# Kernel tuning notes

Measured on AMD Instinct MI355X. Metric: run time of the kernel, lower is better.

## Reference

```python
import jax, jax.numpy as jnp
import numpy as np

N = 262144   # number of samples (graph edges)
D = 32       # in_features; 'delta_t' is column 0
H = D - 1    # hidden width of each bucket MLP
K = 21       # number of time buckets


def setup_inputs() -> dict:
    key = jax.random.key(0)
    ks = jax.random.split(key, 7)
    x = jax.random.uniform(ks[0], (N, D), dtype=jnp.float32)
    x = x.at[:, 0].set(x[:, 0] * 2.1)  # delta_t in (0, 2.1] -> hits all 21 buckets
    s = 1.0 / np.sqrt(H).astype(np.float32)
    a = jax.random.normal(ks[1], (H,), jnp.float32)           # FeatureTransform scale a_i
    b = jax.random.normal(ks[2], (H,), jnp.float32) * 0.1     # FeatureTransform bias b_i
    W1 = jax.random.normal(ks[3], (K, H, H), jnp.float32) * s # layer_blocks weights
    b1 = jax.random.normal(ks[4], (K, H), jnp.float32) * s
    W2 = jax.random.normal(ks[5], (K, H), jnp.float32) * s    # layer_blocks2 weights (out=1)
    b2 = jax.random.normal(ks[6], (K,), jnp.float32) * s
    return {"x": x, "a": a, "b": b, "W1": W1, "b1": b1, "W2": W2, "b2": b2}


def reference(x, a, b, W1, b1, W2, b2):
    # delta_t column is NOT feature-transformed; all other columns are.
    # Note: the torch code mutates x in place, so x_without_t sees the
    # transformed features while t is the raw delta_t.
    t = x[:, 0]                                   # [N]
    feats = x[:, 1:] * a + b                      # FeatureTransform: a_i*x_i + b_i, [N,H]
    # All 21 bucket branches: Linear -> LeakyReLU(0.1) -> Linear(H,1)
    h = jnp.einsum('nd,kde->kne', feats, W1) + b1[:, None, :]   # [K,N,H]
    h = jnp.where(h >= 0, h, 0.1 * h)                           # LeakyReLU(0.1)
    out = jnp.einsum('kne,ke->kn', h, W2) + b2[:, None]         # [K,N]
    # bucket mask: start < t <= end with edges 0.0,0.1,...,2.0,1000
    edges = jnp.concatenate([jnp.arange(K, dtype=jnp.float32) / 10.0,
                             jnp.array([1000.0], dtype=jnp.float32)])
    valid = (t[None, :] > edges[:-1, None]) & (t[None, :] <= edges[1:, None])  # [K,N]
    return (out * valid.astype(out.dtype)).sum(axis=0)[:, None]  # [N,1]
```

## Files before the change

kernel.cpp:

```cpp
#include <hip/hip_runtime.h>
#include <hip/hip_bf16.h>

#define NN 262144
#define DD 32
#define HH 31
#define KK 21
#define ROWS 128
#define FSTRIDE 18

typedef __attribute__((ext_vector_type(8))) short bf16x8;
typedef __attribute__((ext_vector_type(4))) float f32x4;
typedef __attribute__((ext_vector_type(2))) unsigned int u32x2;
typedef __attribute__((ext_vector_type(4))) unsigned int u32x4;

static __device__ __forceinline__ unsigned short f2bf(float f) {
    __hip_bfloat16 h = __float2bfloat16(f);
    return __builtin_bit_cast(unsigned short, h);
}
static __device__ __forceinline__ unsigned pack2(float lo, float hi) {
    return (unsigned)f2bf(lo) | ((unsigned)f2bf(hi) << 16);
}

__global__ __launch_bounds__(64) void prep_kernel(
    const float* __restrict__ W1, const float* __restrict__ b1,
    const float* __restrict__ W2,
    bf16x8* __restrict__ A0tab, bf16x8* __restrict__ A1tab,
    f32x4* __restrict__ cq0b, f32x4* __restrict__ cq0w,
    f32x4* __restrict__ cq1b, f32x4* __restrict__ cq1w)
{
    const int k = (int)blockIdx.x;
    const int lane = (int)threadIdx.x;
    const int lrow = lane & 15, lgrp = lane >> 4;
    const float* __restrict__ W1k = W1 + k * HH * HH;
    const int e0 = lrow, e1 = 16 + lrow;

    bf16x8 A0, A1;
    #pragma unroll
    for (int j = 0; j < 4; ++j) {
        const int d1 = 4 * lgrp + j;
        const int d2 = 16 + 4 * lgrp + j;
        A0[j]     = (short)f2bf(W1k[d1 * HH + e0]);
        A0[4 + j] = (d2 < HH) ? (short)f2bf(W1k[d2 * HH + e0]) : (short)0;
        A1[j]     = (e1 < HH) ? (short)f2bf(W1k[d1 * HH + e1]) : (short)0;
        A1[4 + j] = (e1 < HH && d2 < HH) ? (short)f2bf(W1k[d2 * HH + e1]) : (short)0;
    }
    A0tab[k * 64 + lane] = A0;
    A1tab[k * 64 + lane] = A1;

    f32x4 b0v, w0v, b1v, w1v;
    #pragma unroll
    for (int r = 0; r < 4; ++r) {
        const int e = 4 * lgrp + r, eb = 16 + e;
        b0v[r] = b1[k * HH + e];
        w0v[r] = W2[k * HH + e];
        b1v[r] = (eb < HH) ? b1[k * HH + eb] : 0.0f;
        w1v[r] = (eb < HH) ? W2[k * HH + eb] : 0.0f;
    }
    cq0b[k * 64 + lane] = b0v;
    cq0w[k * 64 + lane] = w0v;
    cq1b[k * 64 + lane] = b1v;
    cq1w[k * 64 + lane] = w1v;
}

__global__ __launch_bounds__(256, 8) void fused_kernel(
    const float* __restrict__ x,
    const float* __restrict__ a,
    const float* __restrict__ b,
    const float* __restrict__ b2,
    const bf16x8* __restrict__ A0tab, const bf16x8* __restrict__ A1tab,
    const f32x4* __restrict__ cq0b, const f32x4* __restrict__ cq0w,
    const f32x4* __restrict__ cq1b, const f32x4* __restrict__ cq1w,
    float* __restrict__ out)
{
    __shared__ unsigned fbf[ROWS * FSTRIDE];
    __shared__ int cnt[KK];
    __shared__ int rnk[KK];
    __shared__ int sbase[KK];
    __shared__ int tstart[KK + 1];
    __shared__ unsigned short sorted[ROWS];

    const int tid = (int)threadIdx.x;
    const int lane = tid & 63;
    const int rowbase = (int)blockIdx.x * ROWS;

    if (tid < KK) { cnt[tid] = 0; rnk[tid] = 0; }
    __syncthreads();

    const int r    = tid >> 1;
    const int half = tid & 1;
    const float4* __restrict__ p =
        reinterpret_cast<const float4*>(x) + (size_t)blockIdx.x * (ROWS * DD / 4) + tid * 4;
    float4 c[4];
    #pragma unroll
    for (int i = 0; i < 4; ++i) c[i] = p[i];

    const float e16 = __shfl(c[0].x, lane + 1);

    const float t = c[0].x;
    const float edges[KK + 1] = {
        0.0f, 0.1f, 0.2f, 0.3f, 0.4f, 0.5f, 0.6f, 0.7f, 0.8f, 0.9f, 1.0f,
        1.1f, 1.2f, 1.3f, 1.4f, 1.5f, 1.6f, 1.7f, 1.8f, 1.9f, 2.0f, 1000.0f
    };
    int kq = -1;
    #pragma unroll
    for (int j = 0; j < KK; ++j)
        if (t > edges[j] && t <= edges[j + 1]) kq = j;

    unsigned* __restrict__ frow = fbf + r * FSTRIDE + half * 8;
    if (half == 0) {
        float f[16];
        #pragma unroll
        for (int j = 0; j < 15; ++j) {
            const float xe = (j + 1 < 4)  ? ((j + 1 == 1) ? c[0].y : (j + 1 == 2) ? c[0].z : c[0].w)
                                          : ((const float*)c)[j + 1];
            f[j] = fmaf(xe, a[j], b[j]);
        }
        f[15] = fmaf(e16, a[15], b[15]);
        #pragma unroll
        for (int s = 0; s < 8; ++s) frow[s] = pack2(f[2 * s], f[2 * s + 1]);
    } else {
        float f[16];
        #pragma unroll
        for (int j = 0; j < 15; ++j) {
            const float xe = ((const float*)c)[j + 1];
            f[j] = fmaf(xe, a[16 + j], b[16 + j]);
        }
        f[15] = 0.0f;
        #pragma unroll
        for (int s = 0; s < 8; ++s) frow[s] = pack2(f[2 * s], f[2 * s + 1]);
    }

    if (half == 0) {
        if (kq >= 0) atomicAdd(&cnt[kq], 1);
        else out[rowbase + r] = 0.0f;
    }
    __syncthreads();

    if (tid < 64) {
        const int j = tid;
        const int c0 = (j < KK) ? cnt[j] : 0;
        const int t0 = (j < KK) ? ((c0 + 15) >> 4) : 0;
        int sc = c0, st = t0;
        #pragma unroll
        for (int off = 1; off < 32; off <<= 1) {
            const int vc = __shfl_up(sc, off);
            const int vt = __shfl_up(st, off);
            if (j >= off) { sc += vc; st += vt; }
        }
        if (j < KK) { sbase[j] = sc - c0; tstart[j] = st - t0; }
        if (j == KK) tstart[KK] = st;
    }
    __syncthreads();
    if (half == 0 && kq >= 0) {
        const int rr = atomicAdd(&rnk[kq], 1);
        sorted[sbase[kq] + rr] = (unsigned short)r;
    }
    __syncthreads();

    const int wave = tid >> 6;
    const int lrow = lane & 15;
    const int lgrp = lane >> 4;

    const int NT = tstart[KK];
    const int ts_l = tstart[(lane <= KK) ? lane : KK];

    for (int tix = wave; tix < NT; tix += 4) {
        const unsigned long long m = __ballot(ts_l <= tix);
        const int k = __builtin_amdgcn_readfirstlane(__popcll(m) - 1);

        const int sb = sbase[k];
        const int cn = cnt[k];
        const int r0 = (tix - tstart[k]) * 16;
        const int rl = r0 + lrow;

        const int R = sorted[sb + ((rl < cn) ? rl : 0)];

        const unsigned* __restrict__ fr = fbf + R * FSTRIDE;
        const u32x2 wlo = *(const u32x2*)(fr + 2 * lgrp);
        const u32x2 whi = *(const u32x2*)(fr + 8 + 2 * lgrp);
        u32x4 bw;
        bw[0] = wlo[0]; bw[1] = wlo[1]; bw[2] = whi[0]; bw[3] = whi[1];
        const bf16x8 B = __builtin_bit_cast(bf16x8, bw);

        const bf16x8 A0 = A0tab[k * 64 + lane];
        const bf16x8 A1 = A1tab[k * 64 + lane];
        const f32x4 cb0 = cq0b[k * 64 + lane];
        const f32x4 cw0 = cq0w[k * 64 + lane];
        const f32x4 cb1 = cq1b[k * 64 + lane];
        const f32x4 cw1 = cq1w[k * 64 + lane];
        const float b2k = b2[k];

        f32x4 acc0 = {0.0f, 0.0f, 0.0f, 0.0f};
        f32x4 acc1 = {0.0f, 0.0f, 0.0f, 0.0f};
        acc0 = __builtin_amdgcn_mfma_f32_16x16x32_bf16(A0, B, acc0, 0, 0, 0);
        acc1 = __builtin_amdgcn_mfma_f32_16x16x32_bf16(A1, B, acc1, 0, 0, 0);

        float S = 0.0f;
        #pragma unroll
        for (int rr = 0; rr < 4; ++rr) {
            const float h0 = acc0[rr] + cb0[rr];
            const float q0 = (h0 >= 0.0f) ? h0 : 0.1f * h0;
            S = fmaf(q0, cw0[rr], S);
            const float h1 = acc1[rr] + cb1[rr];
            const float q1 = (h1 >= 0.0f) ? h1 : 0.1f * h1;
            S = fmaf(q1, cw1[rr], S);
        }
        S += __shfl_xor(S, 16);
        S += __shfl_xor(S, 32);

        if (lgrp == 0 && rl < cn) out[rowbase + R] = S + b2k;
    }
}

extern "C" void kernel_launch(void* const* d_in, const int* in_sizes, int n_in,
                              void* d_out, int out_size, void* d_ws, size_t ws_size,
                              hipStream_t stream) {
    const float* x  = (const float*)d_in[0];
    const float* a  = (const float*)d_in[1];
    const float* b  = (const float*)d_in[2];
    const float* W1 = (const float*)d_in[3];
    const float* b1 = (const float*)d_in[4];
    const float* W2 = (const float*)d_in[5];
    const float* b2 = (const float*)d_in[6];
    float* out = (float*)d_out;

    char* ws = (char*)d_ws;
    bf16x8* A0tab = (bf16x8*)ws;
    bf16x8* A1tab = A0tab + KK * 64;
    f32x4* cq0b = (f32x4*)(A1tab + KK * 64);
    f32x4* cq0w = cq0b + KK * 64;
    f32x4* cq1b = cq0w + KK * 64;
    f32x4* cq1w = cq1b + KK * 64;

    hipLaunchKernelGGL(prep_kernel, dim3(KK), dim3(64), 0, stream,
                       W1, b1, W2, A0tab, A1tab, cq0b, cq0w, cq1b, cq1w);

    hipLaunchKernelGGL(fused_kernel, dim3(NN / ROWS), dim3(256), 0, stream,
                       x, a, b, b2, A0tab, A1tab, cq0b, cq0w, cq1b, cq1w, out);
}
```

Baseline: 22.66 us.

## Stage all bucket weights in LDS per block and double rows per block

The prep kernel now writes a padded bf16 transposed W1 table plus a bias/W2 table. Each fused block copies all 21 buckets' weights (about 48KB) into shared memory and builds its MFMA A fragments from LDS rather than from per-lane global loads. ROWS grows from 128 to 256, so each block sorts and processes twice as many rows, which spreads the weight-staging cost over more work. The catch is much larger LDS use per block (occupancy hint drops to 2), a serial weight copy at block start, and half as many blocks (1024).

```diff
diff --git a/kernel.cpp b/kernel.cpp
--- a/kernel.cpp
+++ b/kernel.cpp
@@ -5,8 +5,12 @@
 #define DD 32
 #define HH 31
 #define KK 21
-#define ROWS 128
+#define ROWS 256
 #define FSTRIDE 18
+#define WROW 36
+#define WK (32 * WROW)
+#define W1BF_B (KK * WK * 2)
+#define BW2_F (KK * 64)
 
 typedef __attribute__((ext_vector_type(8))) short bf16x8;
 typedef __attribute__((ext_vector_type(4))) float f32x4;
@@ -21,58 +25,39 @@
     return (unsigned)f2bf(lo) | ((unsigned)f2bf(hi) << 16);
 }
 
-__global__ __launch_bounds__(64) void prep_kernel(
+__global__ __launch_bounds__(256) void prep_kernel(
     const float* __restrict__ W1, const float* __restrict__ b1,
     const float* __restrict__ W2,
-    bf16x8* __restrict__ A0tab, bf16x8* __restrict__ A1tab,
-    f32x4* __restrict__ cq0b, f32x4* __restrict__ cq0w,
-    f32x4* __restrict__ cq1b, f32x4* __restrict__ cq1w)
+    unsigned short* __restrict__ gW1bf, float* __restrict__ gbw2)
 {
     const int k = (int)blockIdx.x;
-    const int lane = (int)threadIdx.x;
-    const int lrow = lane & 15, lgrp = lane >> 4;
-    const float* __restrict__ W1k = W1 + k * HH * HH;
-    const int e0 = lrow, e1 = 16 + lrow;
-
-    bf16x8 A0, A1;
-    #pragma unroll
-    for (int j = 0; j < 4; ++j) {
-        const int d1 = 4 * lgrp + j;
-        const int d2 = 16 + 4 * lgrp + j;
-        A0[j]     = (short)f2bf(W1k[d1 * HH + e0]);
-        A0[4 + j] = (d2 < HH) ? (short)f2bf(W1k[d2 * HH + e0]) : (short)0;
-        A1[j]     = (e1 < HH) ? (short)f2bf(W1k[d1 * HH + e1]) : (short)0;
-        A1[4 + j] = (e1 < HH && d2 < HH) ? (short)f2bf(W1k[d2 * HH + e1]) : (short)0;
-    }
-    A0tab[k * 64 + lane] = A0;
-    A1tab[k * 64 + lane] = A1;
-
-    f32x4 b0v, w0v, b1v, w1v;
-    #pragma unroll
-    for (int r = 0; r < 4; ++r) {
-        const int e = 4 * lgrp + r, eb = 16 + e;
-        b0v[r] = b1[k * HH + e];
-        w0v[r] = W2[k * HH + e];
-        b1v[r] = (eb < HH) ? b1[k * HH + eb] : 0.0f;
-        w1v[r] = (eb < HH) ? W2[k * HH + eb] : 0.0f;
-    }
-    cq0b[k * 64 + lane] = b0v;
-    cq0w[k * 64 + lane] = w0v;
-    cq1b[k * 64 + lane] = b1v;
-    cq1w[k * 64 + lane] = w1v;
-}
-
-__global__ __launch_bounds__(256, 8) void fused_kernel(
+    const int tid = (int)threadIdx.x;
+    for (int idx = tid; idx < WK; idx += 256) {
+        const int e = idx / WROW, d = idx % WROW;
+        unsigned short v = 0;
+        if (e < HH && d < HH) v = f2bf(W1[k * HH * HH + d * HH + e]);
+        gW1bf[k * WK + idx] = v;
+    }
+    if (tid < 64) {
+        const int e = tid & 31;
+        float v = 0.0f;
+        if (e < HH) v = (tid < 32) ? b1[k * HH + e] : W2[k * HH + e];
+        gbw2[k * 64 + tid] = v;
+    }
+}
+
+__global__ __launch_bounds__(256, 2) void fused_kernel(
     const float* __restrict__ x,
     const float* __restrict__ a,
     const float* __restrict__ b,
     const float* __restrict__ b2,
-    const bf16x8* __restrict__ A0tab, const bf16x8* __restrict__ A1tab,
-    const f32x4* __restrict__ cq0b, const f32x4* __restrict__ cq0w,
-    const f32x4* __restrict__ cq1b, const f32x4* __restrict__ cq1w,
+    const unsigned short* __restrict__ gW1bf,
+    const float* __restrict__ gbw2,
     float* __restrict__ out)
 {
     __shared__ unsigned fbf[ROWS * FSTRIDE];
+    __shared__ __align__(16) unsigned short sW1[KK * WK];
+    __shared__ __align__(16) float sbw2[BW2_F];
     __shared__ int cnt[KK];
     __shared__ int rnk[KK];
     __shared__ int sbase[KK];
@@ -84,55 +69,63 @@
     const int rowbase = (int)blockIdx.x * ROWS;
 
     if (tid < KK) { cnt[tid] = 0; rnk[tid] = 0; }
-    __syncthreads();
-
-    const int r    = tid >> 1;
-    const int half = tid & 1;
-    const float4* __restrict__ p =
-        reinterpret_cast<const float4*>(x) + (size_t)blockIdx.x * (ROWS * DD / 4) + tid * 4;
-    float4 c[4];
-    #pragma unroll
-    for (int i = 0; i < 4; ++i) c[i] = p[i];
-
-    const float e16 = __shfl(c[0].x, lane + 1);
-
-    const float t = c[0].x;
+
+    for (int i = tid; i < W1BF_B / 16; i += 256)
+        ((u32x4*)sW1)[i] = ((const u32x4*)gW1bf)[i];
+    for (int i = tid; i < BW2_F / 4; i += 256)
+        ((f32x4*)sbw2)[i] = ((const f32x4*)gbw2)[i];
+
     const float edges[KK + 1] = {
         0.0f, 0.1f, 0.2f, 0.3f, 0.4f, 0.5f, 0.6f, 0.7f, 0.8f, 0.9f, 1.0f,
         1.1f, 1.2f, 1.3f, 1.4f, 1.5f, 1.6f, 1.7f, 1.8f, 1.9f, 2.0f, 1000.0f
     };
-    int kq = -1;
+    int kq[2] = {-1, -1};
     #pragma unroll
-    for (int j = 0; j < KK; ++j)
-        if (t > edges[j] && t <= edges[j + 1]) kq = j;
-
-    unsigned* __restrict__ frow = fbf + r * FSTRIDE + half * 8;
-    if (half == 0) {
-        float f[16];
+    for (int i = 0; i < 2; ++i) {
+        const int c    = tid + 256 * i;
+        const int row  = c >> 1;
+        const int half = c & 1;
+        const float4* __restrict__ p =
+            reinterpret_cast<const float4*>(x) + (size_t)blockIdx.x * (ROWS * DD / 4) + c * 4;
+        float4 cc[4];
         #pragma unroll
-        for (int j = 0; j < 15; ++j) {
-            const float xe = (j + 1 < 4)  ? ((j + 1 == 1) ? c[0].y : (j + 1 == 2) ? c[0].z : c[0].w)
-                                          : ((const float*)c)[j + 1];
-            f[j] = fmaf(xe, a[j], b[j]);
-        }
-        f[15] = fmaf(e16, a[15], b[15]);
-        #pragma unroll
-        for (int s = 0; s < 8; ++s) frow[s] = pack2(f[2 * s], f[2 * s + 1]);
-    } else {
-        float f[16];
-        #pragma unroll
-        for (int j = 0; j < 15; ++j) {
-            const float xe = ((const float*)c)[j + 1];
-            f[j] = fmaf(xe, a[16 + j], b[16 + j]);
-        }
-        f[15] = 0.0f;
-        #pragma unroll
-        for (int s = 0; s < 8; ++s) frow[s] = pack2(f[2 * s], f[2 * s + 1]);
-    }
-
-    if (half == 0) {
-        if (kq >= 0) atomicAdd(&cnt[kq], 1);
-        else out[rowbase + r] = 0.0f;
+        for (int j = 0; j < 4; ++j) cc[j] = p[j];
+
+        const float e16 = __shfl(cc[0].x, lane + 1);
+        const float t = cc[0].x;
+
+        if (half == 0) {
+            int kk = -1;
+            #pragma unroll
+            for (int j = 0; j < KK; ++j)
+                if (t > edges[j] && t <= edges[j + 1]) kk = j;
+            kq[i] = kk;
+            if (kk >= 0) atomicAdd(&cnt[kk], 1);
+            else out[rowbase + row] = 0.0f;
+        }
+
+        unsigned* __restrict__ frow = fbf + row * FSTRIDE + half * 8;
+        if (half == 0) {
+            float f[16];
+            #pragma unroll
+            for (int j = 0; j < 15; ++j) {
+                const float xe = ((const float*)cc)[j + 1];
+                f[j] = fmaf(xe, a[j], b[j]);
+            }
+            f[15] = fmaf(e16, a[15], b[15]);
+            #pragma unroll
+            for (int s = 0; s < 8; ++s) frow[s] = pack2(f[2 * s], f[2 * s + 1]);
+        } else {
+            float f[16];
+            #pragma unroll
+            for (int j = 0; j < 15; ++j) {
+                const float xe = ((const float*)cc)[j + 1];
+                f[j] = fmaf(xe, a[16 + j], b[16 + j]);
+            }
+            f[15] = 0.0f;
+            #pragma unroll
+            for (int s = 0; s < 8; ++s) frow[s] = pack2(f[2 * s], f[2 * s + 1]);
+        }
     }
     __syncthreads();
 
@@ -151,9 +144,13 @@
         if (j == KK) tstart[KK] = st;
     }
     __syncthreads();
-    if (half == 0 && kq >= 0) {
-        const int rr = atomicAdd(&rnk[kq], 1);
-        sorted[sbase[kq] + rr] = (unsigned short)r;
+    #pragma unroll
+    for (int i = 0; i < 2; ++i) {
+        const int c = tid + 256 * i;
+        if (!(c & 1) && kq[i] >= 0) {
+            const int rr = atomicAdd(&rnk[kq[i]], 1);
+            sorted[sbase[kq[i]] + rr] = (unsigned short)(c >> 1);
+        }
     }
     __syncthreads();
 
@@ -178,16 +175,26 @@
         const unsigned* __restrict__ fr = fbf + R * FSTRIDE;
         const u32x2 wlo = *(const u32x2*)(fr + 2 * lgrp);
         const u32x2 whi = *(const u32x2*)(fr + 8 + 2 * lgrp);
-        u32x4 bw;
-        bw[0] = wlo[0]; bw[1] = wlo[1]; bw[2] = whi[0]; bw[3] = whi[1];
+        u32x4 bw; bw[0] = wlo[0]; bw[1] = wlo[1]; bw[2] = whi[0]; bw[3] = whi[1];
         const bf16x8 B = __builtin_bit_cast(bf16x8, bw);
 
-        const bf16x8 A0 = A0tab[k * 64 + lane];
-        const bf16x8 A1 = A1tab[k * 64 + lane];
-        const f32x4 cb0 = cq0b[k * 64 + lane];
-        const f32x4 cw0 = cq0w[k * 64 + lane];
-        const f32x4 cb1 = cq1b[k * 64 + lane];
-        const f32x4 cw1 = cq1w[k * 64 + lane];
+        const unsigned short* __restrict__ wkp = sW1 + k * WK;
+        const unsigned short* __restrict__ a0p = wkp + lrow * WROW + lgrp * 4;
+        const unsigned short* __restrict__ a1p = a0p + 16 * WROW;
+        const u32x2 alo0 = *(const u32x2*)a0p;
+        const u32x2 ahi0 = *(const u32x2*)(a0p + 16);
+        const u32x2 alo1 = *(const u32x2*)a1p;
+        const u32x2 ahi1 = *(const u32x2*)(a1p + 16);
+        u32x4 aw0; aw0[0] = alo0[0]; aw0[1] = alo0[1]; aw0[2] = ahi0[0]; aw0[3] = ahi0[1];
+        u32x4 aw1; aw1[0] = alo1[0]; aw1[1] = alo1[1]; aw1[2] = ahi1[0]; aw1[3] = ahi1[1];
+        const bf16x8 A0 = __builtin_bit_cast(bf16x8, aw0);
+        const bf16x8 A1 = __builtin_bit_cast(bf16x8, aw1);
+
+        const float* __restrict__ cp = sbw2 + k * 64 + 4 * lgrp;
+        const f32x4 cb0 = *(const f32x4*)cp;
+        const f32x4 cb1 = *(const f32x4*)(cp + 16);
+        const f32x4 cw0 = *(const f32x4*)(cp + 32);
+        const f32x4 cw1 = *(const f32x4*)(cp + 48);
         const float b2k = b2[k];
 
         f32x4 acc0 = {0.0f, 0.0f, 0.0f, 0.0f};
@@ -224,17 +231,12 @@
     const float* b2 = (const float*)d_in[6];
     float* out = (float*)d_out;
 
-    char* ws = (char*)d_ws;
-    bf16x8* A0tab = (bf16x8*)ws;
-    bf16x8* A1tab = A0tab + KK * 64;
-    f32x4* cq0b = (f32x4*)(A1tab + KK * 64);
-    f32x4* cq0w = cq0b + KK * 64;
-    f32x4* cq1b = cq0w + KK * 64;
-    f32x4* cq1w = cq1b + KK * 64;
-
-    hipLaunchKernelGGL(prep_kernel, dim3(KK), dim3(64), 0, stream,
-                       W1, b1, W2, A0tab, A1tab, cq0b, cq0w, cq1b, cq1w);
+    unsigned short* gW1bf = (unsigned short*)d_ws;
+    float* gbw2 = (float*)((char*)d_ws + W1BF_B);
+
+    hipLaunchKernelGGL(prep_kernel, dim3(KK), dim3(256), 0, stream,
+                       W1, b1, W2, gW1bf, gbw2);
 
     hipLaunchKernelGGL(fused_kernel, dim3(NN / ROWS), dim3(256), 0, stream,
-                       x, a, b, b2, A0tab, A1tab, cq0b, cq0w, cq1b, cq1w, out);
-}
+                       x, a, b, b2, gW1bf, gbw2, out);
+}
```

Measured after the change: 29.35 us. 1.3x slower.
